# Optimization experiments

Measured on AMD Instinct MI355X. Metric: run time of the kernel, lower is better.

The kernel has to match this reference:

```python
import math
import jax, jax.numpy as jnp
import numpy as np

D_MODEL = 1024
D_CTX = 1024
NUM_HEADS = 16
ATTN_DIM = 1024
HEAD_DIM = ATTN_DIM // NUM_HEADS  # 64
ROPE_GAMMA = 10.0
ROTARY_BASE = 10000.0
ATTN_SCALE = math.sqrt(ATTN_DIM)  # note: module scales by sqrt(attn_dim), not sqrt(head_dim)


def _apply_rope(x, cos, sin):
    # x: [H,B,T,D]; cos/sin: [1,B,T,D//2]
    half = x.shape[-1] // 2
    x1, x2 = x[..., :half], x[..., half:]
    return jnp.concatenate([x1 * cos - x2 * sin, x1 * sin + x2 * cos], axis=-1)


def setup_inputs() -> dict:
    key = jax.random.key(0)
    ks = jax.random.split(key, 12)
    B, T, L = 4, 1024, 1024
    x = jax.random.normal(ks[0], (B, D_MODEL, T), jnp.float32)
    context = jax.random.normal(ks[1], (B, L, D_CTX), jnp.float32)
    # prefix (padding) masks with per-example valid lengths, as in real padded batches
    lens_q = jnp.array([1024, 896, 768, 640])
    lens_k = jnp.array([1024, 960, 832, 704])
    x_mask = (jnp.arange(T)[None, :] < lens_q[:, None]).astype(jnp.int32)[:, None, :]  # [B,1,T]
    context_mask = (jnp.arange(L)[None, :] < lens_k[:, None]).astype(jnp.int32)[:, None, :]  # [B,1,L]
    s = 0.02
    Wq = jax.random.normal(ks[2], (D_MODEL, ATTN_DIM), jnp.float32) * s
    bq = jax.random.normal(ks[3], (ATTN_DIM,), jnp.float32) * s
    Wk = jax.random.normal(ks[4], (D_CTX, ATTN_DIM), jnp.float32) * s
    bk = jax.random.normal(ks[5], (ATTN_DIM,), jnp.float32) * s
    Wv = jax.random.normal(ks[6], (D_CTX, ATTN_DIM), jnp.float32) * s
    bv = jax.random.normal(ks[7], (ATTN_DIM,), jnp.float32) * s
    Wo = jax.random.normal(ks[8], (ATTN_DIM, D_MODEL), jnp.float32) * s
    bo = jax.random.normal(ks[9], (D_MODEL,), jnp.float32) * s
    return {"x": x, "context": context, "x_mask": x_mask, "context_mask": context_mask,
            "Wq": Wq, "bq": bq, "Wk": Wk, "bk": bk, "Wv": Wv, "bv": bv, "Wo": Wo, "bo": bo}


def reference(x, context, x_mask, context_mask, Wq, bq, Wk, bk, Wv, bv, Wo, bo):
    B, _, T = x.shape
    L = context.shape[1]
    H, D = NUM_HEADS, HEAD_DIM
    xm = x_mask.astype(jnp.float32)          # [B,1,T]
    cmf = context_mask.astype(jnp.float32)   # [B,1,L]

    q = jnp.swapaxes(x, 1, 2) @ Wq + bq      # [B,T,attn_dim]
    k = context @ Wk + bk                    # [B,L,attn_dim]
    v = context @ Wv + bv                    # [B,L,attn_dim]

    q = q.reshape(B, T, H, D).transpose(2, 0, 1, 3)  # [H,B,T,D]
    k = k.reshape(B, L, H, D).transpose(2, 0, 1, 3)  # [H,B,L,D]
    v = v.reshape(B, L, H, D).transpose(2, 0, 1, 3)  # [H,B,L,D]

    # length-normalized RoPE (LARoPE)
    len_q = xm.sum(axis=(-2, -1)).reshape(-1, 1, 1)   # [B,1,1]
    len_k = cmf.sum(axis=(-2, -1)).reshape(-1, 1, 1)  # [B,1,1]
    pos_q = jnp.arange(T, dtype=jnp.float32).reshape(1, -1, 1)
    pos_k = jnp.arange(L, dtype=jnp.float32).reshape(1, -1, 1)
    inv_freq = 1.0 / (ROTARY_BASE ** (jnp.arange(0, D, 2, dtype=jnp.float32) / D))
    theta = (inv_freq * ROPE_GAMMA).reshape(1, 1, -1)  # [1,1,D//2]
    freqs_q = (pos_q / len_q) * theta  # [B,T,D//2]
    freqs_k = (pos_k / len_k) * theta  # [B,L,D//2]
    q = _apply_rope(q, jnp.cos(freqs_q)[None], jnp.sin(freqs_q)[None])
    k = _apply_rope(k, jnp.cos(freqs_k)[None], jnp.sin(freqs_k)[None])

    logits = jnp.einsum('hbtd,hbld->hbtl', q, k) / ATTN_SCALE  # [H,B,T,L]
    key_pad = (context_mask == 0)[None]  # [1,B,1,L]
    logits = jnp.where(key_pad, -jnp.inf, logits)
    attn = jax.nn.softmax(logits, axis=-1)
    query_pad = (x_mask == 0).transpose(1, 0, 2)[..., None]  # [1,B,T,1]
    attn = jnp.where(query_pad, 0.0, attn)

    out = jnp.einsum('hbtl,hbld->hbtd', attn, v)          # [H,B,T,D]
    out = out.transpose(1, 2, 0, 3).reshape(B, T, ATTN_DIM)
    out = out @ Wo + bo                                   # [B,T,d_model]
    out = out * jnp.swapaxes(xm, 1, 2)                    # [B,T,1] broadcast
    return jnp.swapaxes(out, 1, 2)                        # [B,d_model,T]
```

## Files before the change

### kernel.cpp

```cpp
#include <hip/hip_runtime.h>
#include <hip/hip_bf16.h>

typedef __attribute__((ext_vector_type(8))) short s8v;
typedef __attribute__((ext_vector_type(4))) float f4v;
typedef __attribute__((ext_vector_type(4))) unsigned short u4v;
typedef __attribute__((ext_vector_type(2))) unsigned int u2v;

#define NH 16

__device__ __forceinline__ unsigned short f2bf(float f) {
  union { float f; unsigned int u; } v; v.f = f;
  unsigned int r = (v.u + 0x7fffu + ((v.u >> 16) & 1u)) >> 16;
  return (unsigned short)r;
}
__device__ __forceinline__ void gll16(const void* g, void* l) {
  __builtin_amdgcn_global_load_lds((const __attribute__((address_space(1))) void*)g,
                                   (__attribute__((address_space(3))) void*)l, 16, 0, 0);
}
__device__ __forceinline__ unsigned int cvtpk(float lo, float hi) {
  unsigned int r;
  asm volatile("v_cvt_pk_bf16_f32 %0, %1, %2" : "=v"(r) : "v"(lo), "v"(hi));
  return r;
}

__global__ __launch_bounds__(256) void prep_kernel(
    const float* __restrict__ x, const float* __restrict__ ctx,
    const float* __restrict__ Wq, const float* __restrict__ Wk,
    const float* __restrict__ Wv, const float* __restrict__ Wo,
    const int* __restrict__ xm, const int* __restrict__ cm,
    unsigned short* __restrict__ xT, unsigned short* __restrict__ ctxb,
    unsigned short* __restrict__ WqT, unsigned short* __restrict__ WkT,
    unsigned short* __restrict__ WvT, unsigned short* __restrict__ WoT,
    float* __restrict__ lens, float2* __restrict__ rope) {
  const int z = blockIdx.z;
  const int tid = threadIdx.x;
  if (z == 12) {
    if (blockIdx.x | blockIdx.y) return;
    const int w = tid >> 6, lane = tid & 63;
    const int g = w * 2 + (lane >> 5);
    const int l32 = lane & 31;
    const int* m = (g < 4) ? (xm + g * 1024) : (cm + (g - 4) * 1024);
    int s = 0;
    for (int i = l32; i < 1024; i += 32) s += m[i];
    for (int o = 16; o; o >>= 1) s += __shfl_xor(s, o);
    if (l32 == 0) lens[g] = (float)s;
    return;
  }
  if (z == 13) {
    const int idx = blockIdx.y * 32 + blockIdx.x;
    if (idx >= 256) return;
    const int which = idx >> 7;
    const int b = (idx >> 5) & 3;
    const int t0 = (idx & 31) * 32;
    const int* m = (which ? cm : xm) + b * 1024;
    const int lane = tid & 63;
    int s = 0;
    for (int i = lane; i < 1024; i += 64) s += m[i];
    for (int o = 32; o; o >>= 1) s += __shfl_xor(s, o);
    const float len = (float)s;
    const int j = tid & 31;
    const float theta = 10.0f * __expf((float)j * -0.28782313662425572f);
    float2* rt = rope + ((size_t)(which * 4 + b) << 15);
    for (int it = 0; it < 4; ++it) {
      const int t = t0 + (tid >> 5) + it * 8;
      const float fr = (float)t / len * theta;
      float sn, cs;
      __sincosf(fr, &sn, &cs);
      rt[t * 32 + j] = make_float2(cs, sn);
    }
    return;
  }
  if (z >= 8) {
    const float* in = ctx + ((size_t)(z - 8) << 20);
    unsigned short* out = ctxb + ((size_t)(z - 8) << 20);
    const int i = (blockIdx.y * 32 + blockIdx.x) * 1024 + tid * 4;
    const f4v v = *(const f4v*)&in[i];
    u4v o;
#pragma unroll
    for (int j = 0; j < 4; ++j) o[j] = f2bf(v[j]);
    *(u4v*)&out[i] = o;
    return;
  }
  __shared__ unsigned short tile[32][33];
  const float* in;
  unsigned short* out;
  if (z < 4)      { in = x + ((size_t)z << 20); out = xT + ((size_t)z << 20); }
  else if (z == 4){ in = Wq; out = WqT; }
  else if (z == 5){ in = Wk; out = WkT; }
  else if (z == 6){ in = Wv; out = WvT; }
  else            { in = Wo; out = WoT; }
  const int r0 = blockIdx.y * 32, c0 = blockIdx.x * 32;
  const int tx = tid & 31, ty = tid >> 5;
  for (int i = ty; i < 32; i += 8) tile[i][tx] = f2bf(in[(size_t)(r0 + i) * 1024 + c0 + tx]);
  __syncthreads();
  for (int i = ty; i < 32; i += 8) out[(size_t)(c0 + i) * 1024 + r0 + tx] = tile[tx][i];
}

#define STAGE_QKV(buf, kt_) do {                                         \
    const int kn_ = (kt_) * 64;                                          \
    _Pragma("unroll")                                                    \
    for (int i_ = 0; i_ < 4; ++i_) {                                     \
      gll16(Ap + i_ * 32 * 1024 + kn_, &As[buf][(i_ * 256 + tid) * 8]);  \
      gll16(Bp + i_ * 32 * 1024 + kn_, &Bs[buf][(i_ * 256 + tid) * 8]);  \
    }                                                                    \
  } while (0)

__global__ __launch_bounds__(256) void gemm_qkv_kernel(
    const unsigned short* __restrict__ xT, const unsigned short* __restrict__ ctxb,
    const unsigned short* __restrict__ WqT, const unsigned short* __restrict__ WkT,
    const unsigned short* __restrict__ WvT,
    const float* __restrict__ bq, const float* __restrict__ bk, const float* __restrict__ bv,
    unsigned short* __restrict__ Qb, unsigned short* __restrict__ Kb,
    unsigned short* __restrict__ Vtb, const float2* __restrict__ rope,
    const float* __restrict__ lens) {
  __shared__ __attribute__((aligned(16))) unsigned short As[2][8192];
  __shared__ __attribute__((aligned(16))) unsigned short Bs[2][8192];
  const int id = blockIdx.x + (blockIdx.y << 3) + (blockIdx.z << 8);
  const int rest = id >> 3;
  const int my = (id & 7) + ((rest & 3) << 3);
  const int nx = (rest >> 2) & 7;
  const int mode = rest >> 5;
  const int b = my >> 3;
  const int lim = (int)lens[(mode == 0 ? 0 : 4) + b];
  if (((my & 7) << 7) >= lim) return;
  const unsigned short* A  = (mode == 0) ? xT : ctxb;
  const unsigned short* Bt = (mode == 0) ? WqT : (mode == 1) ? WkT : WvT;
  const float* bias        = (mode == 0) ? bq : (mode == 1) ? bk : bv;
  const int tid = threadIdx.x;
  const int lane = tid & 63, w = tid >> 6;
  const int lq = lane & 15, lg = lane >> 4;
  const int m0 = my * 128, n0 = nx * 128;
  const int wm = (w & 1) * 64, wn = (w >> 1) * 64;
  const int cswz = (lq & 7) << 3;
  const int srow = tid >> 3;
  const int scol = ((tid & 7) * 8) ^ ((srow & 7) << 3);
  const unsigned short* Ap = A + (size_t)(m0 + srow) * 1024 + scol;
  const unsigned short* Bp = Bt + (size_t)(n0 + srow) * 1024 + scol;
  f4v acc[4][4] = {};

  STAGE_QKV(0, 0);
  STAGE_QKV(1, 1);

  for (int kt = 0; kt < 16; ++kt) {
    const int cur = kt & 1;
    if (kt < 15) {
      asm volatile("s_waitcnt vmcnt(8)" ::: "memory");
    } else {
      asm volatile("s_waitcnt vmcnt(0)" ::: "memory");
    }
    __builtin_amdgcn_s_barrier();
#pragma unroll
    for (int kc = 0; kc < 2; ++kc) {
      s8v af[4], bfr[4];
#pragma unroll
      for (int i = 0; i < 4; ++i)
        af[i] = *(const s8v*)&As[cur][(wm + i * 16 + lq) * 64 + ((kc * 32 + lg * 8) ^ cswz)];
#pragma unroll
      for (int i = 0; i < 4; ++i)
        bfr[i] = *(const s8v*)&Bs[cur][(wn + i * 16 + lq) * 64 + ((kc * 32 + lg * 8) ^ cswz)];
#pragma unroll
      for (int mi = 0; mi < 4; ++mi)
#pragma unroll
        for (int ni = 0; ni < 4; ++ni)
          acc[mi][ni] = __builtin_amdgcn_mfma_f32_16x16x32_bf16(af[mi], bfr[ni], acc[mi][ni], 0, 0, 0);
    }
    __builtin_amdgcn_s_barrier();
    if (kt + 2 < 16) STAGE_QKV(cur, kt + 2);
  }

  float bv4[4];
#pragma unroll
  for (int ni = 0; ni < 4; ++ni) bv4[ni] = bias[n0 + wn + ni * 16 + lq];

  if (mode <= 1) {
    unsigned short* O = mode ? Kb : Qb;
    const float osc = mode ? 1.0f : 0.0450842200277f;
    const float2* rt = rope + ((size_t)(mode * 4 + b) << 15);
    const int h = (n0 + wn) >> 6;
#pragma unroll
    for (int mi = 0; mi < 4; ++mi) {
#pragma unroll
      for (int rr = 0; rr < 4; ++rr) {
        const int m = m0 + wm + mi * 16 + lg * 4 + rr;
        const int t = m & 1023;
#pragma unroll
        for (int ni = 0; ni < 2; ++ni) {
          const int jj = ni * 16 + lq;
          const float2 cs2 = rt[t * 32 + jj];
          const float x1 = acc[mi][ni][rr] + bv4[ni];
          const float x2 = acc[mi][ni + 2][rr] + bv4[ni + 2];
          unsigned short* bp = &O[((size_t)((b * NH + h) * 1024 + t)) * 64 + jj];
          bp[0] = f2bf((x1 * cs2.x - x2 * cs2.y) * osc);
          bp[32] = f2bf((x1 * cs2.y + x2 * cs2.x) * osc);
        }
      }
    }
  } else {
#pragma unroll
    for (int mi = 0; mi < 4; ++mi) {
      const int mbase = m0 + wm + mi * 16 + lg * 4;
      const int l0 = mbase & 1023;
#pragma unroll
      for (int ni = 0; ni < 4; ++ni) {
        const int n = n0 + wn + ni * 16 + lq;
        const int hh = n >> 6, d = n & 63;
        u4v pk;
#pragma unroll
        for (int rr = 0; rr < 4; ++rr) pk[rr] = f2bf(acc[mi][ni][rr] + bv4[ni]);
        *(u4v*)&Vtb[((size_t)((b * NH + hh) * 64 + d)) * 1024 + l0] = pk;
      }
    }
  }
}

__global__ __launch_bounds__(256) void gemm_o_kernel(
    const unsigned short* __restrict__ A, const unsigned short* __restrict__ Bt,
    const float* __restrict__ bias, float* __restrict__ Cout,
    const int* __restrict__ xmask, const float* __restrict__ lens) {
  __shared__ __attribute__((aligned(16))) unsigned short As[2][8192];
  __shared__ __attribute__((aligned(16))) unsigned short Bs[2][8192];
  const int id = blockIdx.x + (blockIdx.y << 3);
  const int rest = id >> 3;
  const int my = (id & 7) + ((rest & 3) << 3);
  const int nx = rest >> 2;
  const int tid = threadIdx.x;
  const int lane = tid & 63, w = tid >> 6;
  const int lq = lane & 15, lg = lane >> 4;
  const int m0 = my * 128, n0 = nx * 128;
  const int wm = (w & 1) * 64, wn = (w >> 1) * 64;
  const int b = my >> 3;

  if (((my & 7) << 7) >= (int)lens[b]) {
#pragma unroll
    for (int mi = 0; mi < 4; ++mi) {
      const int t0 = (m0 + wm + mi * 16 + lg * 4) & 1023;
      const f4v z = {};
#pragma unroll
      for (int ni = 0; ni < 4; ++ni) {
        const int n = n0 + wn + ni * 16 + lq;
        *(f4v*)&Cout[(size_t)b * 1024 * 1024 + (size_t)n * 1024 + t0] = z;
      }
    }
    return;
  }

  const int cswz = (lq & 7) << 3;
  const int srow = tid >> 3;
  const int scol = ((tid & 7) * 8) ^ ((srow & 7) << 3);
  const unsigned short* Ap = A + (size_t)(m0 + srow) * 1024 + scol;
  const unsigned short* Bp = Bt + (size_t)(n0 + srow) * 1024 + scol;
  f4v acc[4][4] = {};

  STAGE_QKV(0, 0);
  STAGE_QKV(1, 1);

  for (int kt = 0; kt < 16; ++kt) {
    const int cur = kt & 1;
    if (kt < 15) {
      asm volatile("s_waitcnt vmcnt(8)" ::: "memory");
    } else {
      asm volatile("s_waitcnt vmcnt(0)" ::: "memory");
    }
    __builtin_amdgcn_s_barrier();
#pragma unroll
    for (int kc = 0; kc < 2; ++kc) {
      s8v af[4], bfr[4];
#pragma unroll
      for (int i = 0; i < 4; ++i)
        af[i] = *(const s8v*)&As[cur][(wm + i * 16 + lq) * 64 + ((kc * 32 + lg * 8) ^ cswz)];
#pragma unroll
      for (int i = 0; i < 4; ++i)
        bfr[i] = *(const s8v*)&Bs[cur][(wn + i * 16 + lq) * 64 + ((kc * 32 + lg * 8) ^ cswz)];
#pragma unroll
      for (int mi = 0; mi < 4; ++mi)
#pragma unroll
        for (int ni = 0; ni < 4; ++ni)
          acc[mi][ni] = __builtin_amdgcn_mfma_f32_16x16x32_bf16(af[mi], bfr[ni], acc[mi][ni], 0, 0, 0);
    }
    __builtin_amdgcn_s_barrier();
    if (kt + 2 < 16) STAGE_QKV(cur, kt + 2);
  }

  float bv4[4];
#pragma unroll
  for (int ni = 0; ni < 4; ++ni) bv4[ni] = bias[n0 + wn + ni * 16 + lq];
#pragma unroll
  for (int mi = 0; mi < 4; ++mi) {
    const int mbase = m0 + wm + mi * 16 + lg * 4;
    const int t0 = mbase & 1023;
#pragma unroll
    for (int ni = 0; ni < 4; ++ni) {
      const int n = n0 + wn + ni * 16 + lq;
      f4v pk;
#pragma unroll
      for (int rr = 0; rr < 4; ++rr) {
        float v = acc[mi][ni][rr] + bv4[ni];
        v *= (float)xmask[b * 1024 + t0 + rr];
        pk[rr] = v;
      }
      *(f4v*)&Cout[(size_t)b * 1024 * 1024 + (size_t)n * 1024 + t0] = pk;
    }
  }
}

__global__ __launch_bounds__(512) void attn_kernel(
    const unsigned short* __restrict__ Q, const unsigned short* __restrict__ K,
    const unsigned short* __restrict__ Vt, const float* __restrict__ lens,
    unsigned short* __restrict__ Aout) {
  __shared__ __attribute__((aligned(16))) unsigned short Ks[2][4096];
  __shared__ __attribute__((aligned(16))) unsigned short Vs[2][4096];
  __shared__ __attribute__((aligned(16))) unsigned short Plds[8][16][72];
  const int tid = threadIdx.x;
  const int lane = tid & 63, w = tid >> 6;
  const int lq = lane & 15, lg = lane >> 4;
  const int id = blockIdx.x + (blockIdx.y << 3);
  const int bh = (id & 7) + (((id >> 3) & 7) << 3);
  const int qblk = id >> 6;
  const int b = bh >> 4, h = bh & 15;
  const int lenq = (int)lens[b];
  if (qblk * 128 >= lenq) return;
  const int lenk = (int)lens[4 + b];
  const int nkt = (lenk + 63) >> 6;
  const int qrow = qblk * 128 + w * 16;
  const unsigned short* Qp = Q + ((size_t)bh * 1024 + qrow) * 64;
  const unsigned short* Kp = K + (size_t)bh * 65536;
  const unsigned short* Vp = Vt + (size_t)bh * 65536;
  const s8v qf0 = *(const s8v*)&Qp[lq * 64 + lg * 8];
  const s8v qf1 = *(const s8v*)&Qp[lq * 64 + 32 + lg * 8];
  const int r0 = tid >> 3;
  const int c0x = ((tid & 7) * 8) ^ ((r0 & 7) << 3);
  const int cswz = (lq & 7) << 3;

  gll16(&Kp[(size_t)r0 * 64 + c0x], &Ks[0][tid * 8]);
  gll16(&Vp[(size_t)r0 * 1024 + c0x], &Vs[0][tid * 8]);
  __syncthreads();

  float m_run = -1e30f, s_run = 0.0f;
  f4v ot[4] = {};
  for (int kt = 0; kt < nkt; ++kt) {
    const int p = kt & 1;
    if (kt + 1 < nkt) {
      const int kn = (kt + 1) * 64;
      gll16(&Kp[(size_t)(kn + r0) * 64 + c0x], &Ks[p ^ 1][tid * 8]);
      gll16(&Vp[(size_t)r0 * 1024 + kn + c0x], &Vs[p ^ 1][tid * 8]);
    }
    const int k0 = kt * 64;
    const bool full = (k0 + 64 <= lenk);
    float pvv[16];
    float tmax = -1e30f;
    __builtin_amdgcn_s_setprio(1);
#pragma unroll
    for (int kk = 0; kk < 4; ++kk) {
      const int krow = kk * 16 + lq;
      const s8v a0 = *(const s8v*)&Ks[p][krow * 64 + ((lg * 8) ^ cswz)];
      const s8v a1 = *(const s8v*)&Ks[p][krow * 64 + ((32 + lg * 8) ^ cswz)];
      f4v s = {};
      s = __builtin_amdgcn_mfma_f32_16x16x32_bf16(a0, qf0, s, 0, 0, 0);
      s = __builtin_amdgcn_mfma_f32_16x16x32_bf16(a1, qf1, s, 0, 0, 0);
#pragma unroll
      for (int rr = 0; rr < 4; ++rr) {
        float v = s[rr];
        if (!full) {
          const int key = k0 + kk * 16 + lg * 4 + rr;
          if (key >= lenk) v = -1e30f;
        }
        pvv[kk * 4 + rr] = v;
        tmax = fmaxf(tmax, v);
      }
    }
    __builtin_amdgcn_s_setprio(0);
    tmax = fmaxf(tmax, __shfl_xor(tmax, 16));
    tmax = fmaxf(tmax, __shfl_xor(tmax, 32));
    if (__any(tmax > m_run + 8.0f)) {
      const float m_new = fmaxf(m_run, tmax);
      const float alpha = exp2f(m_run - m_new);
#pragma unroll
      for (int d = 0; d < 4; ++d)
#pragma unroll
        for (int j = 0; j < 4; ++j) ot[d][j] *= alpha;
      s_run *= alpha;
      m_run = m_new;
    }
    float psum = 0.0f;
#pragma unroll
    for (int kk = 0; kk < 4; ++kk) {
      const float e0 = exp2f(pvv[kk * 4 + 0] - m_run);
      const float e1 = exp2f(pvv[kk * 4 + 1] - m_run);
      const float e2 = exp2f(pvv[kk * 4 + 2] - m_run);
      const float e3 = exp2f(pvv[kk * 4 + 3] - m_run);
      psum += (e0 + e1) + (e2 + e3);
      u2v pw;
      pw[0] = cvtpk(e0, e1);
      pw[1] = cvtpk(e2, e3);
      *(u2v*)&Plds[w][lq][kk * 16 + lg * 4] = pw;
    }
    psum += __shfl_xor(psum, 16);
    psum += __shfl_xor(psum, 32);
    s_run += psum;
    const s8v pb0 = *(const s8v*)&Plds[w][lq][lg * 8];
    const s8v pb1 = *(const s8v*)&Plds[w][lq][32 + lg * 8];
    __builtin_amdgcn_s_setprio(1);
#pragma unroll
    for (int d = 0; d < 4; ++d) {
      const int vrow = d * 16 + lq;
      const s8v av0 = *(const s8v*)&Vs[p][vrow * 64 + ((lg * 8) ^ cswz)];
      const s8v av1 = *(const s8v*)&Vs[p][vrow * 64 + ((32 + lg * 8) ^ cswz)];
      ot[d] = __builtin_amdgcn_mfma_f32_16x16x32_bf16(av0, pb0, ot[d], 0, 0, 0);
      ot[d] = __builtin_amdgcn_mfma_f32_16x16x32_bf16(av1, pb1, ot[d], 0, 0, 0);
    }
    __builtin_amdgcn_s_setprio(0);
    if (kt + 1 < nkt) __syncthreads();
  }
  const float inv = 1.0f / s_run;
  const int t = qrow + lq;
  unsigned short* op = Aout + ((size_t)(b * 1024 + t)) * 1024 + h * 64;
#pragma unroll
  for (int d = 0; d < 4; ++d) {
    u4v oo;
#pragma unroll
    for (int rr = 0; rr < 4; ++rr) oo[rr] = f2bf(ot[d][rr] * inv);
    *(u4v*)&op[d * 16 + lg * 4] = oo;
  }
}

extern "C" void kernel_launch(void* const* d_in, const int* in_sizes, int n_in,
                              void* d_out, int out_size, void* d_ws, size_t ws_size,
                              hipStream_t stream) {
  const float* x   = (const float*)d_in[0];
  const float* ctx = (const float*)d_in[1];
  const int* xm = (const int*)d_in[2];
  const int* cm = (const int*)d_in[3];
  const float* Wq = (const float*)d_in[4];
  const float* bq = (const float*)d_in[5];
  const float* Wk = (const float*)d_in[6];
  const float* bk = (const float*)d_in[7];
  const float* Wv = (const float*)d_in[8];
  const float* bv = (const float*)d_in[9];
  const float* Wo = (const float*)d_in[10];
  const float* bo = (const float*)d_in[11];

  char* ws = (char*)d_ws;
  const size_t MB = 1024 * 1024;
  unsigned short* xT   = (unsigned short*)(ws);
  unsigned short* AOb  = (unsigned short*)(ws);
  unsigned short* ctxb = (unsigned short*)(ws + 8 * MB);
  unsigned short* WqT  = (unsigned short*)(ws + 16 * MB);
  unsigned short* WkT  = (unsigned short*)(ws + 18 * MB);
  unsigned short* WvT  = (unsigned short*)(ws + 20 * MB);
  unsigned short* WoT  = (unsigned short*)(ws + 22 * MB);
  unsigned short* Qb   = (unsigned short*)(ws + 24 * MB);
  unsigned short* Kb   = (unsigned short*)(ws + 32 * MB);
  unsigned short* Vtb  = (unsigned short*)(ws + 40 * MB);
  float* lens          = (float*)(ws + 48 * MB);
  float2* rope         = (float2*)(ws + 49 * MB);

  prep_kernel<<<dim3(32, 32, 14), 256, 0, stream>>>(x, ctx, Wq, Wk, Wv, Wo, xm, cm,
                                                    xT, ctxb, WqT, WkT, WvT, WoT, lens, rope);
  gemm_qkv_kernel<<<dim3(8, 32, 3), 256, 0, stream>>>(xT, ctxb, WqT, WkT, WvT,
                                                      bq, bk, bv, Qb, Kb, Vtb, rope, lens);
  attn_kernel<<<dim3(8, 64), 512, 0, stream>>>(Qb, Kb, Vtb, lens, AOb);
  gemm_o_kernel<<<dim3(8, 32), 256, 0, stream>>>(AOb, WoT, bo, (float*)d_out, xm, lens);
}
```

Measured before the change: 116.9 us.

## Rewrite attention kernel with 32x32x16 MFMA and in-register P via permlane32 swap

The attention kernel moves from 16x16x32 to 32x32x16 bf16 MFMA. Each wave now handles 32 query rows, and a block runs 4 waves (256 threads) instead of 8. The probability tile is repacked in registers with v_permlane32_swap rather than round-tripped through LDS. Per-row rescale factors and the final normalisers are broadcast through a small LDS array. This cuts LDS traffic and raises MFMA efficiency, at the cost of fewer waves per block, higher register pressure, and scalar 2-byte output stores.

```diff
diff --git a/kernel.cpp b/kernel.cpp
--- a/kernel.cpp
+++ b/kernel.cpp
@@ -3,8 +3,9 @@
 
 typedef __attribute__((ext_vector_type(8))) short s8v;
 typedef __attribute__((ext_vector_type(4))) float f4v;
+typedef __attribute__((ext_vector_type(16))) float f16v;
 typedef __attribute__((ext_vector_type(4))) unsigned short u4v;
-typedef __attribute__((ext_vector_type(2))) unsigned int u2v;
+typedef __attribute__((ext_vector_type(4))) unsigned int u4i;
 
 #define NH 16
 
@@ -22,6 +23,7 @@
   asm volatile("v_cvt_pk_bf16_f32 %0, %1, %2" : "=v"(r) : "v"(lo), "v"(hi));
   return r;
 }
+#define PSWAP(a, b) asm volatile("v_permlane32_swap_b32 %0, %1" : "+v"(a), "+v"(b))
 
 __global__ __launch_bounds__(256) void prep_kernel(
     const float* __restrict__ x, const float* __restrict__ ctx,
@@ -303,16 +305,26 @@
   }
 }
 
-__global__ __launch_bounds__(512) void attn_kernel(
+#define ASTAGE(buf, kt_) do {                                            \
+    const int kn_ = (kt_) * 64;                                          \
+    gll16(&Kp[(size_t)(kn_ + sr) * 64 + scx], &Ks[buf][tid * 8]);        \
+    gll16(&Kp[(size_t)(kn_ + sr + 32) * 64 + scx], &Ks[buf][2048 + tid * 8]); \
+    gll16(&Vp[(size_t)sr * 1024 + kn_ + scx], &Vs[buf][tid * 8]);        \
+    gll16(&Vp[(size_t)(sr + 32) * 1024 + kn_ + scx], &Vs[buf][2048 + tid * 8]); \
+  } while (0)
+
+__global__ __launch_bounds__(256) void attn_kernel(
     const unsigned short* __restrict__ Q, const unsigned short* __restrict__ K,
     const unsigned short* __restrict__ Vt, const float* __restrict__ lens,
     unsigned short* __restrict__ Aout) {
   __shared__ __attribute__((aligned(16))) unsigned short Ks[2][4096];
   __shared__ __attribute__((aligned(16))) unsigned short Vs[2][4096];
-  __shared__ __attribute__((aligned(16))) unsigned short Plds[8][16][72];
+  __shared__ float Ls[4][32];
   const int tid = threadIdx.x;
   const int lane = tid & 63, w = tid >> 6;
-  const int lq = lane & 15, lg = lane >> 4;
+  const int l31 = lane & 31, hi = lane >> 5;
+  const int hi4 = hi * 4, hi8 = hi * 8;
+  const int cswz = (l31 & 7) << 3;
   const int id = blockIdx.x + (blockIdx.y << 3);
   const int bh = (id & 7) + (((id >> 3) & 7) << 3);
   const int qblk = id >> 6;
@@ -321,105 +333,112 @@
   if (qblk * 128 >= lenq) return;
   const int lenk = (int)lens[4 + b];
   const int nkt = (lenk + 63) >> 6;
-  const int qrow = qblk * 128 + w * 16;
-  const unsigned short* Qp = Q + ((size_t)bh * 1024 + qrow) * 64;
+  const int qrow0 = qblk * 128 + w * 32;
+  const unsigned short* Qp = Q + ((size_t)bh * 1024 + qrow0) * 64;
   const unsigned short* Kp = K + (size_t)bh * 65536;
   const unsigned short* Vp = Vt + (size_t)bh * 65536;
-  const s8v qf0 = *(const s8v*)&Qp[lq * 64 + lg * 8];
-  const s8v qf1 = *(const s8v*)&Qp[lq * 64 + 32 + lg * 8];
-  const int r0 = tid >> 3;
-  const int c0x = ((tid & 7) * 8) ^ ((r0 & 7) << 3);
-  const int cswz = (lq & 7) << 3;
-
-  gll16(&Kp[(size_t)r0 * 64 + c0x], &Ks[0][tid * 8]);
-  gll16(&Vp[(size_t)r0 * 1024 + c0x], &Vs[0][tid * 8]);
+  s8v Qf[4];
+#pragma unroll
+  for (int ks = 0; ks < 4; ++ks)
+    Qf[ks] = *(const s8v*)&Qp[l31 * 64 + ks * 16 + hi8];
+  const int sr = tid >> 3;
+  const int scx = ((tid & 7) * 8) ^ ((sr & 7) << 3);
+
+  ASTAGE(0, 0);
   __syncthreads();
 
   float m_run = -1e30f, s_run = 0.0f;
-  f4v ot[4] = {};
+  f16v acc0 = {}, acc1 = {};
   for (int kt = 0; kt < nkt; ++kt) {
     const int p = kt & 1;
-    if (kt + 1 < nkt) {
-      const int kn = (kt + 1) * 64;
-      gll16(&Kp[(size_t)(kn + r0) * 64 + c0x], &Ks[p ^ 1][tid * 8]);
-      gll16(&Vp[(size_t)r0 * 1024 + kn + c0x], &Vs[p ^ 1][tid * 8]);
-    }
+    if (kt + 1 < nkt) ASTAGE(p ^ 1, kt + 1);
     const int k0 = kt * 64;
     const bool full = (k0 + 64 <= lenk);
-    float pvv[16];
+    f16v s0 = {}, s1 = {};
+    __builtin_amdgcn_s_setprio(1);
+#pragma unroll
+    for (int ks = 0; ks < 4; ++ks) {
+      const int c = (ks * 16 + hi8) ^ cswz;
+      const s8v kf0 = *(const s8v*)&Ks[p][l31 * 64 + c];
+      const s8v kf1 = *(const s8v*)&Ks[p][(32 + l31) * 64 + c];
+      s0 = __builtin_amdgcn_mfma_f32_32x32x16_bf16(kf0, Qf[ks], s0, 0, 0, 0);
+      s1 = __builtin_amdgcn_mfma_f32_32x32x16_bf16(kf1, Qf[ks], s1, 0, 0, 0);
+    }
+    __builtin_amdgcn_s_setprio(0);
     float tmax = -1e30f;
-    __builtin_amdgcn_s_setprio(1);
-#pragma unroll
-    for (int kk = 0; kk < 4; ++kk) {
-      const int krow = kk * 16 + lq;
-      const s8v a0 = *(const s8v*)&Ks[p][krow * 64 + ((lg * 8) ^ cswz)];
-      const s8v a1 = *(const s8v*)&Ks[p][krow * 64 + ((32 + lg * 8) ^ cswz)];
-      f4v s = {};
-      s = __builtin_amdgcn_mfma_f32_16x16x32_bf16(a0, qf0, s, 0, 0, 0);
-      s = __builtin_amdgcn_mfma_f32_16x16x32_bf16(a1, qf1, s, 0, 0, 0);
-#pragma unroll
-      for (int rr = 0; rr < 4; ++rr) {
-        float v = s[rr];
-        if (!full) {
-          const int key = k0 + kk * 16 + lg * 4 + rr;
-          if (key >= lenk) v = -1e30f;
-        }
-        pvv[kk * 4 + rr] = v;
-        tmax = fmaxf(tmax, v);
-      }
-    }
-    __builtin_amdgcn_s_setprio(0);
-    tmax = fmaxf(tmax, __shfl_xor(tmax, 16));
+#pragma unroll
+    for (int r = 0; r < 16; ++r) {
+      if (!full) {
+        const int kr = k0 + (r & 3) + 8 * (r >> 2) + hi4;
+        if (kr >= lenk) s0[r] = -1e30f;
+        if (kr + 32 >= lenk) s1[r] = -1e30f;
+      }
+      tmax = fmaxf(tmax, fmaxf(s0[r], s1[r]));
+    }
     tmax = fmaxf(tmax, __shfl_xor(tmax, 32));
     if (__any(tmax > m_run + 8.0f)) {
       const float m_new = fmaxf(m_run, tmax);
       const float alpha = exp2f(m_run - m_new);
-#pragma unroll
-      for (int d = 0; d < 4; ++d)
-#pragma unroll
-        for (int j = 0; j < 4; ++j) ot[d][j] *= alpha;
       s_run *= alpha;
       m_run = m_new;
+      if (hi == 0) Ls[w][l31] = alpha;
+      asm volatile("s_waitcnt lgkmcnt(0)" ::: "memory");
+#pragma unroll
+      for (int r = 0; r < 16; ++r) {
+        const float a = Ls[w][(r & 3) + 8 * (r >> 2) + hi4];
+        acc0[r] *= a;
+        acc1[r] *= a;
+      }
     }
     float psum = 0.0f;
-#pragma unroll
-    for (int kk = 0; kk < 4; ++kk) {
-      const float e0 = exp2f(pvv[kk * 4 + 0] - m_run);
-      const float e1 = exp2f(pvv[kk * 4 + 1] - m_run);
-      const float e2 = exp2f(pvv[kk * 4 + 2] - m_run);
-      const float e3 = exp2f(pvv[kk * 4 + 3] - m_run);
-      psum += (e0 + e1) + (e2 + e3);
-      u2v pw;
-      pw[0] = cvtpk(e0, e1);
-      pw[1] = cvtpk(e2, e3);
-      *(u2v*)&Plds[w][lq][kk * 16 + lg * 4] = pw;
-    }
-    psum += __shfl_xor(psum, 16);
+    float e0v[16], e1v[16];
+#pragma unroll
+    for (int r = 0; r < 16; ++r) {
+      e0v[r] = exp2f(s0[r] - m_run);
+      e1v[r] = exp2f(s1[r] - m_run);
+      psum += e0v[r] + e1v[r];
+    }
     psum += __shfl_xor(psum, 32);
     s_run += psum;
-    const s8v pb0 = *(const s8v*)&Plds[w][lq][lg * 8];
-    const s8v pb1 = *(const s8v*)&Plds[w][lq][32 + lg * 8];
+    s8v pf[4];
+    {
+      unsigned a0 = cvtpk(e0v[0], e0v[1]),   b0 = cvtpk(e0v[4], e0v[5]);
+      unsigned a1 = cvtpk(e0v[2], e0v[3]),   b1 = cvtpk(e0v[6], e0v[7]);
+      unsigned a2 = cvtpk(e0v[8], e0v[9]),   b2 = cvtpk(e0v[12], e0v[13]);
+      unsigned a3 = cvtpk(e0v[10], e0v[11]), b3 = cvtpk(e0v[14], e0v[15]);
+      PSWAP(a0, b0); PSWAP(a1, b1); PSWAP(a2, b2); PSWAP(a3, b3);
+      u4i t0 = {a0, a1, b0, b1}; pf[0] = *(s8v*)&t0;
+      u4i t1 = {a2, a3, b2, b3}; pf[1] = *(s8v*)&t1;
+      unsigned c0 = cvtpk(e1v[0], e1v[1]),   d0 = cvtpk(e1v[4], e1v[5]);
+      unsigned c1 = cvtpk(e1v[2], e1v[3]),   d1 = cvtpk(e1v[6], e1v[7]);
+      unsigned c2 = cvtpk(e1v[8], e1v[9]),   d2 = cvtpk(e1v[12], e1v[13]);
+      unsigned c3 = cvtpk(e1v[10], e1v[11]), d3 = cvtpk(e1v[14], e1v[15]);
+      PSWAP(c0, d0); PSWAP(c1, d1); PSWAP(c2, d2); PSWAP(c3, d3);
+      u4i t2 = {c0, c1, d0, d1}; pf[2] = *(s8v*)&t2;
+      u4i t3 = {c2, c3, d2, d3}; pf[3] = *(s8v*)&t3;
+    }
     __builtin_amdgcn_s_setprio(1);
 #pragma unroll
-    for (int d = 0; d < 4; ++d) {
-      const int vrow = d * 16 + lq;
-      const s8v av0 = *(const s8v*)&Vs[p][vrow * 64 + ((lg * 8) ^ cswz)];
-      const s8v av1 = *(const s8v*)&Vs[p][vrow * 64 + ((32 + lg * 8) ^ cswz)];
-      ot[d] = __builtin_amdgcn_mfma_f32_16x16x32_bf16(av0, pb0, ot[d], 0, 0, 0);
-      ot[d] = __builtin_amdgcn_mfma_f32_16x16x32_bf16(av1, pb1, ot[d], 0, 0, 0);
+    for (int st = 0; st < 4; ++st) {
+      const int c = (st * 16 + hi8) ^ cswz;
+      const s8v vf0 = *(const s8v*)&Vs[p][l31 * 64 + c];
+      const s8v vf1 = *(const s8v*)&Vs[p][(32 + l31) * 64 + c];
+      acc0 = __builtin_amdgcn_mfma_f32_32x32x16_bf16(pf[st], vf0, acc0, 0, 0, 0);
+      acc1 = __builtin_amdgcn_mfma_f32_32x32x16_bf16(pf[st], vf1, acc1, 0, 0, 0);
     }
     __builtin_amdgcn_s_setprio(0);
     if (kt + 1 < nkt) __syncthreads();
   }
   const float inv = 1.0f / s_run;
-  const int t = qrow + lq;
-  unsigned short* op = Aout + ((size_t)(b * 1024 + t)) * 1024 + h * 64;
-#pragma unroll
-  for (int d = 0; d < 4; ++d) {
-    u4v oo;
-#pragma unroll
-    for (int rr = 0; rr < 4; ++rr) oo[rr] = f2bf(ot[d][rr] * inv);
-    *(u4v*)&op[d * 16 + lg * 4] = oo;
+  if (hi == 0) Ls[w][l31] = inv;
+  asm volatile("s_waitcnt lgkmcnt(0)" ::: "memory");
+#pragma unroll
+  for (int r = 0; r < 16; ++r) {
+    const int cr = (r & 3) + 8 * (r >> 2) + hi4;
+    const float iv = Ls[w][cr];
+    unsigned short* op = Aout + ((size_t)(b * 1024 + qrow0 + cr)) * 1024 + h * 64;
+    op[l31] = f2bf(acc0[r] * iv);
+    op[32 + l31] = f2bf(acc1[r] * iv);
   }
 }
 
@@ -458,6 +477,6 @@
                                                     xT, ctxb, WqT, WkT, WvT, WoT, lens, rope);
   gemm_qkv_kernel<<<dim3(8, 32, 3), 256, 0, stream>>>(xT, ctxb, WqT, WkT, WvT,
                                                       bq, bk, bv, Qb, Kb, Vtb, rope, lens);
-  attn_kernel<<<dim3(8, 64), 512, 0, stream>>>(Qb, Kb, Vtb, lens, AOb);
+  attn_kernel<<<dim3(8, 64), 256, 0, stream>>>(Qb, Kb, Vtb, lens, AOb);
   gemm_o_kernel<<<dim3(8, 32), 256, 0, stream>>>(AOb, WoT, bo, (float*)d_out, xm, lens);
 }
```

Result: slower. 173.0 us (+48.0%).

## Read K/V directly from global in attention, dropping LDS staging

Applied to the files above, without the earlier changes.

The attention kernel no longer stages K and V tiles in double-buffered shared memory with async global-to-LDS loads and block barriers. Each wave now loads its MFMA operands straight from global memory, with V loads issued early to overlap the softmax. Blocks shrink from 512 to 256 threads covering 64 query rows, and the grid doubles to match. This removes the barriers and LDS traffic, but every wave now fetches the full K/V tiles itself, and there is no explicit prefetch to hide global latency.

```diff
diff --git a/kernel.cpp b/kernel.cpp
--- a/kernel.cpp
+++ b/kernel.cpp
@@ -303,47 +303,32 @@
   }
 }
 
-__global__ __launch_bounds__(512) void attn_kernel(
+__global__ __launch_bounds__(256) void attn_kernel(
     const unsigned short* __restrict__ Q, const unsigned short* __restrict__ K,
     const unsigned short* __restrict__ Vt, const float* __restrict__ lens,
     unsigned short* __restrict__ Aout) {
-  __shared__ __attribute__((aligned(16))) unsigned short Ks[2][4096];
-  __shared__ __attribute__((aligned(16))) unsigned short Vs[2][4096];
-  __shared__ __attribute__((aligned(16))) unsigned short Plds[8][16][72];
+  __shared__ __attribute__((aligned(16))) unsigned short Plds[4][16][72];
   const int tid = threadIdx.x;
   const int lane = tid & 63, w = tid >> 6;
   const int lq = lane & 15, lg = lane >> 4;
-  const int id = blockIdx.x + (blockIdx.y << 3);
+  const int id = blockIdx.x + (blockIdx.y << 4);
   const int bh = (id & 7) + (((id >> 3) & 7) << 3);
   const int qblk = id >> 6;
   const int b = bh >> 4, h = bh & 15;
   const int lenq = (int)lens[b];
-  if (qblk * 128 >= lenq) return;
+  if (qblk * 64 >= lenq) return;
   const int lenk = (int)lens[4 + b];
   const int nkt = (lenk + 63) >> 6;
-  const int qrow = qblk * 128 + w * 16;
+  const int qrow = qblk * 64 + w * 16;
   const unsigned short* Qp = Q + ((size_t)bh * 1024 + qrow) * 64;
   const unsigned short* Kp = K + (size_t)bh * 65536;
   const unsigned short* Vp = Vt + (size_t)bh * 65536;
   const s8v qf0 = *(const s8v*)&Qp[lq * 64 + lg * 8];
   const s8v qf1 = *(const s8v*)&Qp[lq * 64 + 32 + lg * 8];
-  const int r0 = tid >> 3;
-  const int c0x = ((tid & 7) * 8) ^ ((r0 & 7) << 3);
-  const int cswz = (lq & 7) << 3;
-
-  gll16(&Kp[(size_t)r0 * 64 + c0x], &Ks[0][tid * 8]);
-  gll16(&Vp[(size_t)r0 * 1024 + c0x], &Vs[0][tid * 8]);
-  __syncthreads();
 
   float m_run = -1e30f, s_run = 0.0f;
   f4v ot[4] = {};
   for (int kt = 0; kt < nkt; ++kt) {
-    const int p = kt & 1;
-    if (kt + 1 < nkt) {
-      const int kn = (kt + 1) * 64;
-      gll16(&Kp[(size_t)(kn + r0) * 64 + c0x], &Ks[p ^ 1][tid * 8]);
-      gll16(&Vp[(size_t)r0 * 1024 + kn + c0x], &Vs[p ^ 1][tid * 8]);
-    }
     const int k0 = kt * 64;
     const bool full = (k0 + 64 <= lenk);
     float pvv[16];
@@ -351,9 +336,9 @@
     __builtin_amdgcn_s_setprio(1);
 #pragma unroll
     for (int kk = 0; kk < 4; ++kk) {
-      const int krow = kk * 16 + lq;
-      const s8v a0 = *(const s8v*)&Ks[p][krow * 64 + ((lg * 8) ^ cswz)];
-      const s8v a1 = *(const s8v*)&Ks[p][krow * 64 + ((32 + lg * 8) ^ cswz)];
+      const unsigned short* kp = Kp + (size_t)(k0 + kk * 16 + lq) * 64 + lg * 8;
+      const s8v a0 = *(const s8v*)kp;
+      const s8v a1 = *(const s8v*)(kp + 32);
       f4v s = {};
       s = __builtin_amdgcn_mfma_f32_16x16x32_bf16(a0, qf0, s, 0, 0, 0);
       s = __builtin_amdgcn_mfma_f32_16x16x32_bf16(a1, qf1, s, 0, 0, 0);
@@ -369,6 +354,13 @@
       }
     }
     __builtin_amdgcn_s_setprio(0);
+    s8v av0[4], av1[4];
+#pragma unroll
+    for (int d = 0; d < 4; ++d) {
+      const unsigned short* vp = Vp + (size_t)(d * 16 + lq) * 1024 + k0 + lg * 8;
+      av0[d] = *(const s8v*)vp;
+      av1[d] = *(const s8v*)(vp + 32);
+    }
     tmax = fmaxf(tmax, __shfl_xor(tmax, 16));
     tmax = fmaxf(tmax, __shfl_xor(tmax, 32));
     if (__any(tmax > m_run + 8.0f)) {
@@ -402,14 +394,10 @@
     __builtin_amdgcn_s_setprio(1);
 #pragma unroll
     for (int d = 0; d < 4; ++d) {
-      const int vrow = d * 16 + lq;
-      const s8v av0 = *(const s8v*)&Vs[p][vrow * 64 + ((lg * 8) ^ cswz)];
-      const s8v av1 = *(const s8v*)&Vs[p][vrow * 64 + ((32 + lg * 8) ^ cswz)];
-      ot[d] = __builtin_amdgcn_mfma_f32_16x16x32_bf16(av0, pb0, ot[d], 0, 0, 0);
-      ot[d] = __builtin_amdgcn_mfma_f32_16x16x32_bf16(av1, pb1, ot[d], 0, 0, 0);
+      ot[d] = __builtin_amdgcn_mfma_f32_16x16x32_bf16(av0[d], pb0, ot[d], 0, 0, 0);
+      ot[d] = __builtin_amdgcn_mfma_f32_16x16x32_bf16(av1[d], pb1, ot[d], 0, 0, 0);
     }
     __builtin_amdgcn_s_setprio(0);
-    if (kt + 1 < nkt) __syncthreads();
   }
   const float inv = 1.0f / s_run;
   const int t = qrow + lq;
@@ -458,6 +446,6 @@
                                                     xT, ctxb, WqT, WkT, WvT, WoT, lens, rope);
   gemm_qkv_kernel<<<dim3(8, 32, 3), 256, 0, stream>>>(xT, ctxb, WqT, WkT, WvT,
                                                       bq, bk, bv, Qb, Kb, Vtb, rope, lens);
-  attn_kernel<<<dim3(8, 64), 512, 0, stream>>>(Qb, Kb, Vtb, lens, AOb);
+  attn_kernel<<<dim3(16, 64), 256, 0, stream>>>(Qb, Kb, Vtb, lens, AOb);
   gemm_o_kernel<<<dim3(8, 32), 256, 0, stream>>>(AOb, WoT, bo, (float*)d_out, xm, lens);
 }
```

New measurement: 191.5 us. 63.8% more time.
